# Performance work log

Measured on AMD Instinct MI355X. Metric: run time of the kernel, lower is better.

Reference implementation:

```python
import jax, jax.numpy as jnp
import numpy as np

STRIDE, PAD, DIL, DG, GROUPS = 1, 1, 1, 1, 1


def setup_inputs() -> dict:
    key = jax.random.key(0)
    k1, k2, k3, k4 = jax.random.split(key, 4)
    B, Cin, H, W = 4, 64, 128, 128
    Cout, kh, kw = 64, 3, 3
    x = jax.random.normal(k1, (B, Cin, H, W), jnp.float32)
    # learned offsets: [B, dg*2*kh*kw, Ho, Wo], interleaved (y, x) per kernel tap
    offset = jax.random.normal(k2, (B, DG * 2 * kh * kw, H, W), jnp.float32)
    # modulation mask: [B, dg*kh*kw, Ho, Wo] in (0,1) (sigmoid applied upstream in DCNv2 packs)
    mask = jax.random.uniform(k3, (B, DG * kh * kw, H, W), jnp.float32)
    stdv = 1.0 / np.sqrt(Cin * kh * kw)
    weight = jax.random.uniform(k4, (Cout, Cin // GROUPS, kh, kw), jnp.float32, -stdv, stdv)
    bias = jnp.zeros((Cout,), jnp.float32)
    return {"x": x, "offset": offset, "mask": mask, "weight": weight, "bias": bias}


def reference(x, offset, mask, weight, bias):
    B, Cin, H, W = x.shape
    Cout, _, kh, kw = weight.shape
    K2 = kh * kw
    Ho = (H + 2 * PAD - DIL * (kh - 1) - 1) // STRIDE + 1
    Wo = (W + 2 * PAD - DIL * (kw - 1) - 1) // STRIDE + 1
    Cg = Cin // DG

    # base sampling grid per kernel tap: [K2, Ho, Wo]
    ky = (jnp.arange(kh) * DIL).repeat(kw)          # [K2]
    kx = jnp.tile(jnp.arange(kw) * DIL, kh)          # [K2]
    base_y = jnp.arange(Ho) * STRIDE - PAD           # [Ho]
    base_x = jnp.arange(Wo) * STRIDE - PAD           # [Wo]
    grid_y = ky[:, None, None] + base_y[None, :, None]  # [K2, Ho, 1]
    grid_x = kx[:, None, None] + base_x[None, None, :]  # [K2, 1, Wo]

    # offsets: [B, dg, K2, 2, Ho, Wo] with channel 0=y, 1=x (DCNv2 interleaving)
    off = offset.reshape(B, DG, K2, 2, Ho, Wo)
    py = grid_y[None, None].astype(x.dtype) + off[:, :, :, 0]  # [B, dg, K2, Ho, Wo]
    px = grid_x[None, None].astype(x.dtype) + off[:, :, :, 1]

    y0 = jnp.floor(py).astype(jnp.int32)
    x0 = jnp.floor(px).astype(jnp.int32)
    ly = py - y0.astype(x.dtype)
    lx = px - x0.astype(x.dtype)

    xg = x.reshape(B, DG, Cg, H * W)

    def gather(iy, ix):
        valid = ((iy >= 0) & (iy < H) & (ix >= 0) & (ix < W)).astype(x.dtype)
        idx = jnp.clip(iy, 0, H - 1) * W + jnp.clip(ix, 0, W - 1)   # [B, dg, K2, Ho, Wo]
        flat = idx.reshape(B, DG, 1, -1)
        vals = jnp.take_along_axis(xg, flat, axis=3)                 # [B, dg, Cg, K2*Ho*Wo]
        return vals.reshape(B, DG, Cg, K2, Ho, Wo) * valid[:, :, None]

    w00 = ((1 - ly) * (1 - lx))[:, :, None]
    w01 = ((1 - ly) * lx)[:, :, None]
    w10 = (ly * (1 - lx))[:, :, None]
    w11 = (ly * lx)[:, :, None]

    sampled = (gather(y0, x0) * w00 + gather(y0, x0 + 1) * w01
               + gather(y0 + 1, x0) * w10 + gather(y0 + 1, x0 + 1) * w11)
    sampled = sampled * mask.reshape(B, DG, 1, K2, Ho, Wo)

    # im2col GEMM (groups=1): [B, Cin*K2, Ho*Wo] x [Cout, Cin*K2]
    cols = sampled.reshape(B, Cin * K2, Ho * Wo)
    wf = weight.reshape(Cout, Cin * K2)
    out = jnp.einsum('ok,bkp->bop', wf, cols).reshape(B, Cout, Ho, Wo)
    return out + bias[None, :, None, None]
```

## Files before the change

### kernel.cpp

```cpp
#include <hip/hip_runtime.h>
#include <math.h>

#define H_    128
#define W_    128
#define HW_   (H_ * W_)
#define CIN_  64
#define COUT_ 64
#define K2_   9
#define B_    4
#define NROWS 10
#define LDS_BYTES (NROWS * 128 * 128)

typedef __bf16 bf16x8 __attribute__((ext_vector_type(8)));
typedef __bf16 bf16x4 __attribute__((ext_vector_type(4)));
typedef float  f32x4  __attribute__((ext_vector_type(4)));

__global__ __launch_bounds__(256) void wtrans3_kernel(const float* __restrict__ w,
                                                      __bf16* __restrict__ wt3) {
    int idx = blockIdx.x * 256 + threadIdx.x;
    if (idx >= K2_ * 2 * 4 * 64 * 8) return;
    int e    = idx & 7;
    int lane = (idx >> 3) & 63;
    int ct   = (idx >> 9) & 3;
    int s    = (idx >> 11) & 1;
    int k    = idx >> 12;
    int co   = ct * 16 + (lane & 15);
    int cin  = s * 32 + (lane >> 4) * 8 + e;
    wt3[idx] = (__bf16)w[(co * CIN_ + cin) * K2_ + k];
}

__global__ __launch_bounds__(1024, 4) void dcn_lds_kernel(
    const float* __restrict__ x,
    const float* __restrict__ offset,
    const float* __restrict__ mask,
    const __bf16* __restrict__ wt3,
    const float* __restrict__ bias,
    float* __restrict__ out)
{
    extern __shared__ char sm[];

    const int tid  = threadIdx.x;
    const int wave = tid >> 6;
    const int lane = tid & 63;
    const int n16  = lane & 15;
    const int kb   = lane >> 4;

    const int bid0 = blockIdx.x;
    const int bidx = (bid0 & 7) * 32 + (bid0 >> 3);
    const int b   = bidx >> 6;
    const int ho0 = (bidx & 63) * 2;

    const float* xb = x + (size_t)b * CIN_ * HW_;

    {
        const int g5     = tid >> 5;
        const int px4    = tid & 31;
        const int rowpar = g5 >> 4;
        const int c0     = (g5 & 15) * 4;
        const int chunk  = c0 >> 3;
        const int eoff   = (c0 & 7) * 2;
#pragma unroll
        for (int it = 0; it < 5; ++it) {
            const int r = it * 2 + rowpar;
            const int srow = min(max(ho0 - 4 + r, 0), H_ - 1);
            const float* g = xb + ((size_t)c0 * H_ + srow) * W_ + px4 * 4;
            const float4 v0 = *(const float4*)(g);
            const float4 v1 = *(const float4*)(g + HW_);
            const float4 v2 = *(const float4*)(g + 2 * HW_);
            const float4 v3 = *(const float4*)(g + 3 * HW_);
            const float* f0 = (const float*)&v0;
            const float* f1 = (const float*)&v1;
            const float* f2 = (const float*)&v2;
            const float* f3 = (const float*)&v3;
#pragma unroll
            for (int e = 0; e < 4; ++e) {
                const int px = px4 * 4 + e;
                const int q  = (chunk + px + (px >> 3)) & 7;
                bf16x4 pk;
                pk[0] = (__bf16)f0[e];
                pk[1] = (__bf16)f1[e];
                pk[2] = (__bf16)f2[e];
                pk[3] = (__bf16)f3[e];
                *(bf16x4*)(sm + (((size_t)r * 128 + px) * 8 + q) * 16 + eoff) = pk;
            }
        }
    }
    __syncthreads();

    const int rr  = wave >> 3;
    const int til = wave & 7;
    const int ho  = ho0 + rr;
    const int wos = til * 16 + n16;
    const int pix = ho * W_ + wos;
    const float* offb = offset + (size_t)b * (2 * K2_) * HW_ + pix;
    const float* mb   = mask   + (size_t)b * K2_ * HW_ + pix;

    f32x4 acc[4];
#pragma unroll
    for (int t = 0; t < 4; ++t) acc[t] = (f32x4){0.f, 0.f, 0.f, 0.f};

    float oy = offb[0];
    float ox = offb[HW_];
    float mm = mb[0];

    unsigned flags = 0;

#pragma unroll 3
    for (int k = 0; k < K2_; ++k) {
        const int ky = k / 3, kx = k % 3;
        const float py  = (float)(ho - 1 + ky) + oy;
        const float pxf = (float)(wos - 1 + kx) + ox;
        const float fy = floorf(py), fx = floorf(pxf);
        const int   y0 = (int)fy,    x0 = (int)fx;
        const float ly = py - fy,    lx = pxf - fx;

        const bool vy0 = (y0 >= 0) && (y0 < H_);
        const bool vy1 = (y0 + 1 >= 0) && (y0 + 1 < H_);
        const float vx0 = (x0 >= 0 && x0 < W_)         ? 1.f : 0.f;
        const float vx1 = (x0 + 1 >= 0 && x0 + 1 < W_) ? 1.f : 0.f;
        const int cy0 = min(max(y0, 0), H_ - 1);
        const int cy1 = min(max(y0 + 1, 0), H_ - 1);
        const int cx0 = min(max(x0, 0), W_ - 1);
        const int cx1 = min(max(x0 + 1, 0), W_ - 1);

        const int s0 = cy0 - ho0 + 4;
        const int s1 = cy1 - ho0 + 4;
        const bool win0 = ((unsigned)s0 <= 9u);
        const bool win1 = ((unsigned)s1 <= 9u);
        const int s0c = min(max(s0, 0), 9);
        const int s1c = min(max(s1, 0), 9);

        const float a0  = (vy0 && win0) ? mm * (1.f - ly) : 0.f;
        const float a1  = (vy1 && win1) ? mm * ly         : 0.f;
        const float l0x = (1.f - lx) * vx0;
        const float l1x = lx * vx1;
        const float W00 = a0 * l0x, W01 = a0 * l1x;
        const float W10 = a1 * l0x, W11 = a1 * l1x;

        flags |= ((vy0 && !win0) || (vy1 && !win1)) ? (1u << k) : 0u;

        const int key0 = cx0 + (cx0 >> 3);
        const int key1 = cx1 + (cx1 >> 3);
        const char* r00 = sm + ((size_t)(s0c * 128 + cx0) * 8) * 16;
        const char* r01 = sm + ((size_t)(s0c * 128 + cx1) * 8) * 16;
        const char* r10 = sm + ((size_t)(s1c * 128 + cx0) * 8) * 16;
        const char* r11 = sm + ((size_t)(s1c * 128 + cx1) * 8) * 16;

        const bf16x8 a00 = *(const bf16x8*)(r00 + (((kb     + key0) & 7) << 4));
        const bf16x8 c00 = *(const bf16x8*)(r00 + (((kb + 4 + key0) & 7) << 4));
        const bf16x8 a01 = *(const bf16x8*)(r01 + (((kb     + key1) & 7) << 4));
        const bf16x8 c01 = *(const bf16x8*)(r01 + (((kb + 4 + key1) & 7) << 4));
        const bf16x8 a10 = *(const bf16x8*)(r10 + (((kb     + key0) & 7) << 4));
        const bf16x8 c10 = *(const bf16x8*)(r10 + (((kb + 4 + key0) & 7) << 4));
        const bf16x8 a11 = *(const bf16x8*)(r11 + (((kb     + key1) & 7) << 4));
        const bf16x8 c11 = *(const bf16x8*)(r11 + (((kb + 4 + key1) & 7) << 4));

        if (k + 1 < K2_) {
            oy = offb[(2 * (k + 1)) * HW_];
            ox = offb[(2 * (k + 1) + 1) * HW_];
            mm = mb[(k + 1) * HW_];
        }

        bf16x8 bf0, bf1;
#pragma unroll
        for (int e = 0; e < 8; ++e) {
            const float v0 = W00 * (float)a00[e] + W01 * (float)a01[e]
                           + W10 * (float)a10[e] + W11 * (float)a11[e];
            const float v1 = W00 * (float)c00[e] + W01 * (float)c01[e]
                           + W10 * (float)c10[e] + W11 * (float)c11[e];
            bf0[e] = (__bf16)v0;
            bf1[e] = (__bf16)v1;
        }

        const __bf16* wk = wt3 + (size_t)k * (2 * 4 * 64 * 8);
#pragma unroll
        for (int ct = 0; ct < 4; ++ct) {
            const bf16x8 A0 = *(const bf16x8*)(wk + (0 * 4 + ct) * 512 + lane * 8);
            const bf16x8 A1 = *(const bf16x8*)(wk + (1 * 4 + ct) * 512 + lane * 8);
            acc[ct] = __builtin_amdgcn_mfma_f32_16x16x32_bf16(A0, bf0, acc[ct], 0, 0, 0);
            acc[ct] = __builtin_amdgcn_mfma_f32_16x16x32_bf16(A1, bf1, acc[ct], 0, 0, 0);
        }
    }

    if (__any((int)flags)) {
#pragma unroll 1
        for (int k = 0; k < K2_; ++k) {
            if (!__any((int)(flags & (1u << k)))) continue;
            const float oyf = offb[(2 * k) * HW_];
            const float oxf = offb[(2 * k + 1) * HW_];
            const float mmf = mb[k * HW_];
            const int ky = k / 3, kx = k % 3;
            const float py  = (float)(ho - 1 + ky) + oyf;
            const float pxf = (float)(wos - 1 + kx) + oxf;
            const float fy = floorf(py), fx = floorf(pxf);
            const int   y0 = (int)fy,    x0 = (int)fx;
            const float ly = py - fy,    lx = pxf - fx;

            const bool vy0 = (y0 >= 0) && (y0 < H_);
            const bool vy1 = (y0 + 1 >= 0) && (y0 + 1 < H_);
            const float vx0 = (x0 >= 0 && x0 < W_)         ? 1.f : 0.f;
            const float vx1 = (x0 + 1 >= 0 && x0 + 1 < W_) ? 1.f : 0.f;
            const int cy0 = min(max(y0, 0), H_ - 1);
            const int cy1 = min(max(y0 + 1, 0), H_ - 1);
            const int cx0 = min(max(x0, 0), W_ - 1);
            const int cx1 = min(max(x0 + 1, 0), W_ - 1);
            const bool win0 = ((unsigned)(cy0 - ho0 + 4) <= 9u);
            const bool win1 = ((unsigned)(cy1 - ho0 + 4) <= 9u);
            const bool needF0 = vy0 && !win0;
            const bool needF1 = vy1 && !win1;

            const float a0f = needF0 ? mmf * (1.f - ly) : 0.f;
            const float a1f = needF1 ? mmf * ly         : 0.f;
            const float l0x = (1.f - lx) * vx0;
            const float l1x = lx * vx1;
            const float W00f = a0f * l0x, W01f = a0f * l1x;
            const float W10f = a1f * l0x, W11f = a1f * l1x;

            const __bf16* wk = wt3 + (size_t)k * (2 * 4 * 64 * 8);
#pragma unroll
            for (int half = 0; half < 2; ++half) {
                const int cinb = half * 32 + kb * 8;
                float g00[8], g01[8], g10[8], g11[8];
#pragma unroll
                for (int e = 0; e < 8; ++e) { g00[e] = g01[e] = g10[e] = g11[e] = 0.f; }
                if (needF0) {
                    const float* gl = xb + (size_t)cinb * HW_ + (size_t)cy0 * W_;
#pragma unroll
                    for (int e = 0; e < 8; ++e) {
                        g00[e] = gl[(size_t)e * HW_ + cx0];
                        g01[e] = gl[(size_t)e * HW_ + cx1];
                    }
                }
                if (needF1) {
                    const float* gl = xb + (size_t)cinb * HW_ + (size_t)cy1 * W_;
#pragma unroll
                    for (int e = 0; e < 8; ++e) {
                        g10[e] = gl[(size_t)e * HW_ + cx0];
                        g11[e] = gl[(size_t)e * HW_ + cx1];
                    }
                }
                bf16x8 bfF;
#pragma unroll
                for (int e = 0; e < 8; ++e)
                    bfF[e] = (__bf16)(W00f * g00[e] + W01f * g01[e]
                                    + W10f * g10[e] + W11f * g11[e]);
#pragma unroll
                for (int ct = 0; ct < 4; ++ct) {
                    const bf16x8 A = *(const bf16x8*)(wk + (half * 4 + ct) * 512 + lane * 8);
                    acc[ct] = __builtin_amdgcn_mfma_f32_16x16x32_bf16(A, bfF, acc[ct], 0, 0, 0);
                }
            }
        }
    }

#pragma unroll
    for (int ct = 0; ct < 4; ++ct) {
#pragma unroll
        for (int r = 0; r < 4; ++r) {
            const int co = ct * 16 + kb * 4 + r;
            out[((size_t)(b * COUT_ + co)) * HW_ + pix] = acc[ct][r] + bias[co];
        }
    }
}

extern "C" void kernel_launch(void* const* d_in, const int* in_sizes, int n_in,
                              void* d_out, int out_size, void* d_ws, size_t ws_size,
                              hipStream_t stream) {
    const float* x      = (const float*)d_in[0];
    const float* offset = (const float*)d_in[1];
    const float* mask   = (const float*)d_in[2];
    const float* weight = (const float*)d_in[3];
    const float* bias   = (const float*)d_in[4];
    float* out = (float*)d_out;
    __bf16* wt3 = (__bf16*)d_ws;

    hipFuncSetAttribute(reinterpret_cast<const void*>(dcn_lds_kernel),
                        hipFuncAttributeMaxDynamicSharedMemorySize, LDS_BYTES);

    wtrans3_kernel<<<(K2_ * 2 * 4 * 64 * 8 + 255) / 256, 256, 0, stream>>>(weight, wt3);
    dcn_lds_kernel<<<B_ * H_ / 2, 1024, LDS_BYTES, stream>>>(x, offset, mask, wt3, bias, out);
}
```

Before: 33.70 us.

## Move bilinear interpolation after the MFMA by running one GEMM per corner

Instead of blending the four bilinear corner samples on the vector ALU into one bf16 column before the MFMA, the kernel now runs separate MFMA pairs on each raw corner sample and scales each 16x16 result by that corner's per-pixel weight when accumulating. This removes the per-element bf16-to-float conversions, FMAs and repacking, and the rounding of the blended value. In exchange it quadruples the MFMA count and adds scaled-accumulate vector work per corner. The unroll factor drops from 3 to 2, probably to limit register pressure.

```diff
diff --git a/kernel.cpp b/kernel.cpp
--- a/kernel.cpp
+++ b/kernel.cpp
@@ -98,6 +98,7 @@
     f32x4 acc[4];
 #pragma unroll
     for (int t = 0; t < 4; ++t) acc[t] = (f32x4){0.f, 0.f, 0.f, 0.f};
+    const f32x4 Z = (f32x4){0.f, 0.f, 0.f, 0.f};
 
     float oy = offb[0];
     float ox = offb[HW_];
@@ -105,7 +106,7 @@
 
     unsigned flags = 0;
 
-#pragma unroll 3
+#pragma unroll 2
     for (int k = 0; k < K2_; ++k) {
         const int ky = k / 3, kx = k % 3;
         const float py  = (float)(ho - 1 + ky) + oy;
@@ -145,15 +146,17 @@
         const char* r01 = sm + ((size_t)(s0c * 128 + cx1) * 8) * 16;
         const char* r10 = sm + ((size_t)(s1c * 128 + cx0) * 8) * 16;
         const char* r11 = sm + ((size_t)(s1c * 128 + cx1) * 8) * 16;
-
-        const bf16x8 a00 = *(const bf16x8*)(r00 + (((kb     + key0) & 7) << 4));
-        const bf16x8 c00 = *(const bf16x8*)(r00 + (((kb + 4 + key0) & 7) << 4));
-        const bf16x8 a01 = *(const bf16x8*)(r01 + (((kb     + key1) & 7) << 4));
-        const bf16x8 c01 = *(const bf16x8*)(r01 + (((kb + 4 + key1) & 7) << 4));
-        const bf16x8 a10 = *(const bf16x8*)(r10 + (((kb     + key0) & 7) << 4));
-        const bf16x8 c10 = *(const bf16x8*)(r10 + (((kb + 4 + key0) & 7) << 4));
-        const bf16x8 a11 = *(const bf16x8*)(r11 + (((kb     + key1) & 7) << 4));
-        const bf16x8 c11 = *(const bf16x8*)(r11 + (((kb + 4 + key1) & 7) << 4));
+        const int o00 = ((kb + key0) & 7) << 4;
+        const int o01 = ((kb + key1) & 7) << 4;
+
+        const bf16x8 B00l = *(const bf16x8*)(r00 + o00);
+        const bf16x8 B00h = *(const bf16x8*)(r00 + (o00 ^ 64));
+        const bf16x8 B01l = *(const bf16x8*)(r01 + o01);
+        const bf16x8 B01h = *(const bf16x8*)(r01 + (o01 ^ 64));
+        const bf16x8 B10l = *(const bf16x8*)(r10 + o00);
+        const bf16x8 B10h = *(const bf16x8*)(r10 + (o00 ^ 64));
+        const bf16x8 B11l = *(const bf16x8*)(r11 + o01);
+        const bf16x8 B11h = *(const bf16x8*)(r11 + (o01 ^ 64));
 
         if (k + 1 < K2_) {
             oy = offb[(2 * (k + 1)) * HW_];
@@ -161,24 +164,24 @@
             mm = mb[(k + 1) * HW_];
         }
 
-        bf16x8 bf0, bf1;
-#pragma unroll
-        for (int e = 0; e < 8; ++e) {
-            const float v0 = W00 * (float)a00[e] + W01 * (float)a01[e]
-                           + W10 * (float)a10[e] + W11 * (float)a11[e];
-            const float v1 = W00 * (float)c00[e] + W01 * (float)c01[e]
-                           + W10 * (float)c10[e] + W11 * (float)c11[e];
-            bf0[e] = (__bf16)v0;
-            bf1[e] = (__bf16)v1;
-        }
-
         const __bf16* wk = wt3 + (size_t)k * (2 * 4 * 64 * 8);
 #pragma unroll
         for (int ct = 0; ct < 4; ++ct) {
             const bf16x8 A0 = *(const bf16x8*)(wk + (0 * 4 + ct) * 512 + lane * 8);
             const bf16x8 A1 = *(const bf16x8*)(wk + (1 * 4 + ct) * 512 + lane * 8);
-            acc[ct] = __builtin_amdgcn_mfma_f32_16x16x32_bf16(A0, bf0, acc[ct], 0, 0, 0);
-            acc[ct] = __builtin_amdgcn_mfma_f32_16x16x32_bf16(A1, bf1, acc[ct], 0, 0, 0);
+            f32x4 D;
+            D = __builtin_amdgcn_mfma_f32_16x16x32_bf16(A0, B00l, Z, 0, 0, 0);
+            D = __builtin_amdgcn_mfma_f32_16x16x32_bf16(A1, B00h, D, 0, 0, 0);
+            acc[ct] += W00 * D;
+            D = __builtin_amdgcn_mfma_f32_16x16x32_bf16(A0, B01l, Z, 0, 0, 0);
+            D = __builtin_amdgcn_mfma_f32_16x16x32_bf16(A1, B01h, D, 0, 0, 0);
+            acc[ct] += W01 * D;
+            D = __builtin_amdgcn_mfma_f32_16x16x32_bf16(A0, B10l, Z, 0, 0, 0);
+            D = __builtin_amdgcn_mfma_f32_16x16x32_bf16(A1, B10h, D, 0, 0, 0);
+            acc[ct] += W10 * D;
+            D = __builtin_amdgcn_mfma_f32_16x16x32_bf16(A0, B11l, Z, 0, 0, 0);
+            D = __builtin_amdgcn_mfma_f32_16x16x32_bf16(A1, B11h, D, 0, 0, 0);
+            acc[ct] += W11 * D;
         }
     }
 
```

New measurement: 42.63 us. 1.26x slower.
